# Kernel optimization log

Hardware: AMD Instinct MI355X
Metric: run time of the kernel (lower is better)

## Reference

```python
import jax, jax.numpy as jnp
import numpy as np

B, N, D, K, S = 16, 1024, 256, 16, 512
TEMP = 0.5   # self.temperature, set externally in the repo
EPS = 1e-10


def _gumbel(key, shape):
    u = jax.random.uniform(key, shape, dtype=jnp.float32)
    return -jnp.log(-jnp.log(u + EPS) + EPS)


def setup_inputs() -> dict:
    key = jax.random.key(0)
    k1, k2, k3 = jax.random.split(key, 3)
    return {
        "ze": jax.random.normal(k1, (B, N, D), dtype=jnp.float32),
        "c_logits": jax.random.normal(k2, (B, K), dtype=jnp.float32),
        "books": jax.random.normal(k3, (K, S, D), dtype=jnp.float32),
        "log_param_q": jnp.asarray(np.log(0.5), dtype=jnp.float32),
        "log_param_q_cls": jnp.asarray(np.log(0.5), dtype=jnp.float32),
        "is_train": 1,
    }


def reference(ze, c_logits, books, log_param_q, log_param_q_cls, is_train):
    # training-path forward of GaussianVectorQuantizer
    param_q = 1.0 + jnp.exp(log_param_q)
    precision_q = 0.5 / jnp.clip(param_q, 1e-10)
    param_q_cls = 1.0 + jnp.exp(log_param_q_cls)
    precision_q_cls = 0.5 / jnp.clip(param_q_cls, 1e-10)

    gkey = jax.random.key(42)
    kg1, kg2 = jax.random.split(gkey)

    # gumbel-softmax over clusters: (B, K)
    c_probs = jax.nn.softmax(
        (c_logits * precision_q_cls + _gumbel(kg1, c_logits.shape)) / TEMP, axis=-1
    )

    # pairwise squared distances to every codebook entry of every cluster: (B, N, K, S)
    z2 = jnp.sum(ze * ze, axis=-1)[:, :, None, None]          # (B, N, 1, 1)
    b2 = jnp.sum(books * books, axis=-1)[None, None]          # (1, 1, K, S)
    cross = jnp.einsum('bnd,ksd->bnks', ze, books)            # (B, N, K, S)
    logit_all = -(z2 - 2.0 * cross + b2) * precision_q        # (B, N, K, S)

    # cluster-probability-weighted logits: (B, N, S)
    logits = jnp.einsum('bnks,bk->bns', logit_all, c_probs)

    # gumbel-softmax encodings per cluster, then weighted codebook matmul
    enc = jax.nn.softmax((logit_all + _gumbel(kg2, logit_all.shape)) / TEMP, axis=-1)
    zq = jnp.einsum('bnks,ksd,bk->bnd', enc, books, c_probs)  # (B, N, D)

    prob = jax.nn.softmax(logits, axis=-1)
    log_prob = jax.nn.log_softmax(logits, axis=-1)
    return zq, precision_q, prob, log_prob
```

## Files before the change

kernel.cpp:

```cpp
#include <hip/hip_runtime.h>
#include <cstdint>
#include <cstddef>

#define JAX_PARTITIONABLE 1

namespace {

constexpr int Bsz = 16, Nn = 1024, Dd = 256, Kk = 16, Ss = 512;
constexpr uint32_t BN = (uint32_t)Bsz * Nn;
constexpr int ZQ_SIZE = Bsz * Nn * Dd;
constexpr int PQ_OFF = ZQ_SIZE;
constexpr int PROB_OFF = ZQ_SIZE + 1;
constexpr int BNS = Bsz * Nn * Ss;
constexpr int LP_OFF = PROB_OFF + BNS;

constexpr int WS_CP = 0;
constexpr int WS_B2 = 256;
constexpr int WS_WB2 = WS_B2 + Kk * Ss;
constexpr int WS_WBF = WS_WB2 + Bsz * Ss;
constexpr int WS_BBF = WS_WBF + Bsz * Ss * Dd;
constexpr int WS_BTF = WS_BBF + (Kk * Ss * Dd) / 2;

typedef __attribute__((ext_vector_type(8))) short bf16x8;
typedef __attribute__((ext_vector_type(4))) short short4v;
typedef __attribute__((ext_vector_type(4))) float f32x4;

struct KP { uint32_t a, b; };

__host__ __device__ constexpr KP tf2x32(uint32_t k0, uint32_t k1,
                                        uint32_t x0, uint32_t x1) {
  uint32_t ks[3] = {k0, k1, k0 ^ k1 ^ 0x1BD11BDAu};
  const int rot[2][4] = {{13, 15, 26, 6}, {17, 29, 16, 24}};
  x0 += ks[0];
  x1 += ks[1];
#pragma unroll
  for (int i = 0; i < 5; ++i) {
#pragma unroll
    for (int j = 0; j < 4; ++j) {
      int r = rot[i & 1][j];
      x0 += x1;
      x1 = (x1 << r) | (x1 >> (32 - r));
      x1 ^= x0;
    }
    x0 += ks[(i + 1) % 3];
    x1 += ks[(i + 2) % 3] + (uint32_t)(i + 1);
  }
  return {x0, x1};
}

#if JAX_PARTITIONABLE
constexpr KP KG1 = tf2x32(0u, 42u, 0u, 0u);
constexpr KP KG2 = tf2x32(0u, 42u, 0u, 1u);
#else
constexpr KP KH0 = tf2x32(0u, 42u, 0u, 2u);
constexpr KP KH1 = tf2x32(0u, 42u, 1u, 3u);
constexpr KP KG1 = {KH0.a, KH1.a};
constexpr KP KG2 = {KH0.b, KH1.b};
#endif

__device__ __forceinline__ float jax_gumbel(KP key, uint32_t idx, uint32_t half) {
#if JAX_PARTITIONABLE
  (void)half;
  KP h = tf2x32(key.a, key.b, 0u, idx);
  uint32_t bits = h.a ^ h.b;
#else
  uint32_t lo = idx < half ? idx : idx - half;
  KP h = tf2x32(key.a, key.b, lo, lo + half);
  uint32_t bits = idx < half ? h.a : h.b;
#endif
  float u = __uint_as_float((bits >> 9) | 0x3F800000u) - 1.0f;
  return -__logf(-__logf(u + 1e-10f) + 1e-10f);
}

__device__ __forceinline__ float prec_q(const float* p) {
  return 0.5f / fmaxf(1.0f + expf(p[0]), 1e-10f);
}

__device__ __forceinline__ short f2bf(float x) {
  uint32_t u = __float_as_uint(x);
  uint32_t r = (u + 0x7FFFu + ((u >> 16) & 1u)) >> 16;
  return (short)r;
}

__global__ void __launch_bounds__(256) cprobs_kernel(
    const float* __restrict__ c_logits, const float* __restrict__ lpq,
    const float* __restrict__ lpq_cls, float* __restrict__ ws,
    float* __restrict__ out) {
  __shared__ float sl[256];
  const int t = threadIdx.x;
  const float pqc = prec_q(lpq_cls);
  float g = jax_gumbel(KG1, (uint32_t)t, 128u);
  sl[t] = (c_logits[t] * pqc + g) * 2.0f;
  __syncthreads();
  const int b = t >> 4;
  float m = -3.0e38f;
  for (int j = 0; j < 16; ++j) m = fmaxf(m, sl[b * 16 + j]);
  float sum = 0.f;
  for (int j = 0; j < 16; ++j) sum += expf(sl[b * 16 + j] - m);
  ws[WS_CP + t] = expf(sl[t] - m) / sum;
  if (t == 0) out[PQ_OFF] = prec_q(lpq);
}

__global__ void __launch_bounds__(256) norms_kernel(
    const float* __restrict__ books, float* __restrict__ ws) {
  const int row = blockIdx.x * 4 + (threadIdx.x >> 6);
  const int lane = threadIdx.x & 63;
  float4 v = ((const float4*)(books + (size_t)row * Dd))[lane];
  float s = v.x * v.x + v.y * v.y + v.z * v.z + v.w * v.w;
#pragma unroll
  for (int d = 1; d < 64; d <<= 1) s += __shfl_xor(s, d);
  if (lane == 0) ws[WS_B2 + row] = s;
}

__global__ void __launch_bounds__(256) prep_kernel(
    const float* __restrict__ books, float* __restrict__ ws) {
  __shared__ short tile[16 * 256];
  const int k = blockIdx.x >> 5;
  const int s0 = (blockIdx.x & 31) << 4;
  short* bbf = (short*)(ws + WS_BBF);
  short* btf = (short*)(ws + WS_BTF);
  const int t = threadIdx.x;
#pragma unroll
  for (int i = 0; i < 4; ++i) {
    int idx = t + 256 * i;
    int r = idx >> 6, dq = idx & 63;
    float4 v = ((const float4*)books)[(size_t)(k * Ss + s0 + r) * 64 + dq];
    short4v h = {f2bf(v.x), f2bf(v.y), f2bf(v.z), f2bf(v.w)};
    *(short4v*)&bbf[(size_t)(k * Ss + s0 + r) * 256 + dq * 4] = h;
    *(short4v*)&tile[r * 256 + dq * 4] = h;
  }
  __syncthreads();
  const int d = t;
  short vals[16];
#pragma unroll
  for (int r = 0; r < 16; ++r) vals[r] = tile[r * 256 + d];
  bf16x8 lo, hi;
#pragma unroll
  for (int r = 0; r < 8; ++r) { lo[r] = vals[r]; hi[r] = vals[r + 8]; }
  size_t base = ((size_t)(k * 256 + d)) * 512 + s0;
  *(bf16x8*)&btf[base] = lo;
  *(bf16x8*)&btf[base + 8] = hi;
}

__global__ void __launch_bounds__(256) wbooks_kernel(
    const float* __restrict__ books, float* __restrict__ ws) {
  const int bs = blockIdx.x;
  const int b = bs >> 9, s = bs & 511;
  const int d = threadIdx.x;
  const float* cp = ws + WS_CP + b * 16;
  float acc = 0.f;
#pragma unroll
  for (int k = 0; k < 16; ++k)
    acc = fmaf(cp[k], books[((size_t)(k * Ss + s)) * Dd + d], acc);
  short* wbf = (short*)(ws + WS_WBF);
  wbf[((size_t)(b * Ss + s)) * Dd + d] = f2bf(acc);
  if (d == 0) {
    float a2 = 0.f;
#pragma unroll
    for (int k = 0; k < 16; ++k) a2 = fmaf(cp[k], ws[WS_B2 + k * Ss + s], a2);
    ws[WS_WB2 + b * Ss + s] = a2;
  }
}

__global__ void __launch_bounds__(512, 4) mlogits_kernel(
    const float* __restrict__ ze, const float* __restrict__ lpq,
    const float* __restrict__ ws, float* __restrict__ out) {
  __shared__ short ze_s[32 * 264];
  __shared__ float2 redms[32][9];
  const int b = blockIdx.x >> 5;
  const int n0 = (blockIdx.x & 31) << 5;
  const int t = threadIdx.x;
  const int w = t >> 6, lane = t & 63, c = lane & 15, q = lane >> 4;
  const float pq = prec_q(lpq);
  const short* wbf = (const short*)(ws + WS_WBF);
  const float* wb2 = ws + WS_WB2;

#pragma unroll
  for (int i = 0; i < 4; ++i) {
    int idx = t + 512 * i;
    int r = idx >> 6, dq = idx & 63;
    float4 v = ((const float4*)ze)[(size_t)(b * Nn + n0 + r) * 64 + dq];
    short4v h = {f2bf(v.x), f2bf(v.y), f2bf(v.z), f2bf(v.w)};
    *(short4v*)&ze_s[r * 264 + dq * 4] = h;
  }
  __syncthreads();

  f32x4 acc1[2][4];
#pragma unroll
  for (int rt = 0; rt < 2; ++rt)
#pragma unroll
    for (int st = 0; st < 4; ++st) acc1[rt][st] = (f32x4)(0.f);
  for (int dstep = 0; dstep < 8; ++dstep) {
    bf16x8 a0 = *(const bf16x8*)&ze_s[(c) * 264 + dstep * 32 + q * 8];
    bf16x8 a1 = *(const bf16x8*)&ze_s[(16 + c) * 264 + dstep * 32 + q * 8];
#pragma unroll
    for (int st = 0; st < 4; ++st) {
      bf16x8 bB = *(const bf16x8*)&wbf[((size_t)(b * Ss + w * 64 + st * 16 + c)) * 256 +
                                       dstep * 32 + q * 8];
      acc1[0][st] = __builtin_amdgcn_mfma_f32_16x16x32_bf16(a0, bB, acc1[0][st], 0, 0, 0);
      acc1[1][st] = __builtin_amdgcn_mfma_f32_16x16x32_bf16(a1, bB, acc1[1][st], 0, 0, 0);
    }
  }

  float mx[2][4], sm[2][4];
#pragma unroll
  for (int rt = 0; rt < 2; ++rt)
#pragma unroll
    for (int reg = 0; reg < 4; ++reg) mx[rt][reg] = -3.0e38f;
#pragma unroll
  for (int st = 0; st < 4; ++st) {
    const float wb2v = wb2[b * Ss + w * 64 + st * 16 + c];
#pragma unroll
    for (int rt = 0; rt < 2; ++rt)
#pragma unroll
      for (int reg = 0; reg < 4; ++reg) {
        float v = (2.f * acc1[rt][st][reg] - wb2v) * pq;
        acc1[rt][st][reg] = v;
        mx[rt][reg] = fmaxf(mx[rt][reg], v);
      }
  }
#pragma unroll
  for (int m = 1; m < 16; m <<= 1)
#pragma unroll
    for (int rt = 0; rt < 2; ++rt)
#pragma unroll
      for (int reg = 0; reg < 4; ++reg)
        mx[rt][reg] = fmaxf(mx[rt][reg], __shfl_xor(mx[rt][reg], m));
#pragma unroll
  for (int rt = 0; rt < 2; ++rt)
#pragma unroll
    for (int reg = 0; reg < 4; ++reg) sm[rt][reg] = 0.f;
#pragma unroll
  for (int st = 0; st < 4; ++st)
#pragma unroll
    for (int rt = 0; rt < 2; ++rt)
#pragma unroll
      for (int reg = 0; reg < 4; ++reg)
        sm[rt][reg] += __expf(acc1[rt][st][reg] - mx[rt][reg]);
#pragma unroll
  for (int m = 1; m < 16; m <<= 1)
#pragma unroll
    for (int rt = 0; rt < 2; ++rt)
#pragma unroll
      for (int reg = 0; reg < 4; ++reg) sm[rt][reg] += __shfl_xor(sm[rt][reg], m);
  if (c == 0) {
#pragma unroll
    for (int rt = 0; rt < 2; ++rt)
#pragma unroll
      for (int reg = 0; reg < 4; ++reg)
        redms[rt * 16 + q * 4 + reg][w] = make_float2(mx[rt][reg], sm[rt][reg]);
  }
  __syncthreads();

#pragma unroll
  for (int rt = 0; rt < 2; ++rt)
#pragma unroll
    for (int reg = 0; reg < 4; ++reg) {
      int rl = rt * 16 + q * 4 + reg;
      float M = mx[rt][reg];
#pragma unroll
      for (int w2 = 0; w2 < 8; ++w2) M = fmaxf(M, redms[rl][w2].x);
      float T = 0.f;
#pragma unroll
      for (int w2 = 0; w2 < 8; ++w2)
        T = fmaf(redms[rl][w2].y, __expf(redms[rl][w2].x - M), T);
      const float invT = __builtin_amdgcn_rcpf(T);
      const float lT = __logf(T);
      const size_t base = (size_t)(b * Nn + n0 + rl) * Ss;
#pragma unroll
      for (int st = 0; st < 4; ++st) {
        int s = w * 64 + st * 16 + c;
        float v = acc1[rt][st][reg] - M;
        out[PROB_OFF + base + s] = __expf(v) * invT;
        out[LP_OFF + base + s] = v - lT;
      }
    }
}

__global__ void __launch_bounds__(512, 4) zq_kernel(
    const float* __restrict__ ze, const float* __restrict__ lpq,
    const float* __restrict__ ws, float* __restrict__ out) {
  __shared__ short ze_s[32 * 264];
  __shared__ short enc_s[32 * 520];
  __shared__ float2 redms[32][9];
  __shared__ float cpk[16];

  const int b = blockIdx.x >> 5;
  const int n0 = (blockIdx.x & 31) << 5;
  const int t = threadIdx.x;
  const int w = t >> 6, lane = t & 63, c = lane & 15, q = lane >> 4;
  const float pq = prec_q(lpq);
  const short* bbf = (const short*)(ws + WS_BBF);
  const short* btf = (const short*)(ws + WS_BTF);
  const float* b2p = ws + WS_B2;

  if (t < 16) cpk[t] = ws[WS_CP + b * 16 + t];
#pragma unroll
  for (int i = 0; i < 4; ++i) {
    int idx = t + 512 * i;
    int r = idx >> 6, dq = idx & 63;
    float4 v = ((const float4*)ze)[(size_t)(b * Nn + n0 + r) * 64 + dq];
    short4v h = {f2bf(v.x), f2bf(v.y), f2bf(v.z), f2bf(v.w)};
    *(short4v*)&ze_s[r * 264 + dq * 4] = h;
  }
  __syncthreads();

  f32x4 acc2[2][2];
#pragma unroll
  for (int rt = 0; rt < 2; ++rt)
#pragma unroll
    for (int dt = 0; dt < 2; ++dt) acc2[rt][dt] = (f32x4)(0.f);

  for (int k = 0; k < 16; ++k) {
    f32x4 acc1[2][4];
#pragma unroll
    for (int rt = 0; rt < 2; ++rt)
#pragma unroll
      for (int st = 0; st < 4; ++st) acc1[rt][st] = (f32x4)(0.f);
    for (int dstep = 0; dstep < 8; ++dstep) {
      bf16x8 a0 = *(const bf16x8*)&ze_s[(c) * 264 + dstep * 32 + q * 8];
      bf16x8 a1 = *(const bf16x8*)&ze_s[(16 + c) * 264 + dstep * 32 + q * 8];
#pragma unroll
      for (int st = 0; st < 4; ++st) {
        bf16x8 bB = *(const bf16x8*)&bbf[((size_t)(k * Ss + w * 64 + st * 16 + c)) * 256 +
                                         dstep * 32 + q * 8];
        acc1[0][st] = __builtin_amdgcn_mfma_f32_16x16x32_bf16(a0, bB, acc1[0][st], 0, 0, 0);
        acc1[1][st] = __builtin_amdgcn_mfma_f32_16x16x32_bf16(a1, bB, acc1[1][st], 0, 0, 0);
      }
    }

    float b2v[4];
#pragma unroll
    for (int st = 0; st < 4; ++st) b2v[st] = b2p[k * Ss + w * 64 + st * 16 + c];
    float mx[2][4], sm[2][4];
#pragma unroll
    for (int rt = 0; rt < 2; ++rt)
#pragma unroll
      for (int reg = 0; reg < 4; ++reg) mx[rt][reg] = -3.0e38f;
#pragma unroll
    for (int rt = 0; rt < 2; ++rt)
#pragma unroll
      for (int st = 0; st < 4; ++st)
#pragma unroll
        for (int reg = 0; reg < 4; ++reg) {
          int row = n0 + rt * 16 + q * 4 + reg;
          uint32_t gi = ((uint32_t)(b * Nn + row) * (uint32_t)Kk + (uint32_t)k) * (uint32_t)Ss +
                        (uint32_t)(w * 64 + st * 16 + c);
          float g = jax_gumbel(KG2, gi, 0u);
          float v = ((2.f * acc1[rt][st][reg] - b2v[st]) * pq + g) * 2.f;
          acc1[rt][st][reg] = v;
          mx[rt][reg] = fmaxf(mx[rt][reg], v);
        }
#pragma unroll
    for (int m = 1; m < 16; m <<= 1)
#pragma unroll
      for (int rt = 0; rt < 2; ++rt)
#pragma unroll
        for (int reg = 0; reg < 4; ++reg)
          mx[rt][reg] = fmaxf(mx[rt][reg], __shfl_xor(mx[rt][reg], m));
#pragma unroll
    for (int rt = 0; rt < 2; ++rt)
#pragma unroll
      for (int reg = 0; reg < 4; ++reg) sm[rt][reg] = 0.f;
#pragma unroll
    for (int rt = 0; rt < 2; ++rt)
#pragma unroll
      for (int st = 0; st < 4; ++st)
#pragma unroll
        for (int reg = 0; reg < 4; ++reg) {
          float e = __expf(acc1[rt][st][reg] - mx[rt][reg]);
          acc1[rt][st][reg] = e;
          sm[rt][reg] += e;
        }
#pragma unroll
    for (int m = 1; m < 16; m <<= 1)
#pragma unroll
      for (int rt = 0; rt < 2; ++rt)
#pragma unroll
        for (int reg = 0; reg < 4; ++reg) sm[rt][reg] += __shfl_xor(sm[rt][reg], m);
    if (c == 0) {
#pragma unroll
      for (int rt = 0; rt < 2; ++rt)
#pragma unroll
        for (int reg = 0; reg < 4; ++reg) {
          int rl = rt * 16 + q * 4 + reg;
          redms[rl][w] = make_float2(mx[rt][reg], sm[rt][reg]);
        }
    }
    __syncthreads();

    const float cpv = cpk[k];
#pragma unroll
    for (int rt = 0; rt < 2; ++rt)
#pragma unroll
      for (int reg = 0; reg < 4; ++reg) {
        int rl = rt * 16 + q * 4 + reg;
        float M = mx[rt][reg];
#pragma unroll
        for (int w2 = 0; w2 < 8; ++w2) M = fmaxf(M, redms[rl][w2].x);
        float T = 0.f;
#pragma unroll
        for (int w2 = 0; w2 < 8; ++w2)
          T = fmaf(redms[rl][w2].y, __expf(redms[rl][w2].x - M), T);
        float scale = cpv * __expf(mx[rt][reg] - M) * __builtin_amdgcn_rcpf(T);
#pragma unroll
        for (int st = 0; st < 4; ++st)
          enc_s[rl * 520 + w * 64 + st * 16 + c] = f2bf(acc1[rt][st][reg] * scale);
      }
    __syncthreads();

    for (int ss = 0; ss < 16; ++ss) {
      bf16x8 a0 = *(const bf16x8*)&enc_s[(c) * 520 + ss * 32 + q * 8];
      bf16x8 a1 = *(const bf16x8*)&enc_s[(16 + c) * 520 + ss * 32 + q * 8];
#pragma unroll
      for (int dt = 0; dt < 2; ++dt) {
        bf16x8 bB = *(const bf16x8*)&btf[((size_t)(k * 256 + w * 32 + dt * 16 + c)) * 512 +
                                         ss * 32 + q * 8];
        acc2[0][dt] = __builtin_amdgcn_mfma_f32_16x16x32_bf16(a0, bB, acc2[0][dt], 0, 0, 0);
        acc2[1][dt] = __builtin_amdgcn_mfma_f32_16x16x32_bf16(a1, bB, acc2[1][dt], 0, 0, 0);
      }
    }
  }

#pragma unroll
  for (int rt = 0; rt < 2; ++rt)
#pragma unroll
    for (int dt = 0; dt < 2; ++dt)
#pragma unroll
      for (int reg = 0; reg < 4; ++reg) {
        int row = n0 + rt * 16 + q * 4 + reg;
        int d = w * 32 + dt * 16 + c;
        out[(size_t)(b * Nn + row) * Dd + d] = acc2[rt][dt][reg];
      }
}

}

extern "C" void kernel_launch(void* const* d_in, const int* in_sizes, int n_in,
                              void* d_out, int out_size, void* d_ws, size_t ws_size,
                              hipStream_t stream) {
  (void)in_sizes; (void)n_in; (void)out_size; (void)ws_size;
  const float* ze = (const float*)d_in[0];
  const float* c_logits = (const float*)d_in[1];
  const float* books = (const float*)d_in[2];
  const float* lpq = (const float*)d_in[3];
  const float* lpq_cls = (const float*)d_in[4];
  float* out = (float*)d_out;
  float* ws = (float*)d_ws;

  hipLaunchKernelGGL(cprobs_kernel, dim3(1), dim3(256), 0, stream,
                     c_logits, lpq, lpq_cls, ws, out);
  hipLaunchKernelGGL(norms_kernel, dim3(Kk * Ss / 4), dim3(256), 0, stream, books, ws);
  hipLaunchKernelGGL(prep_kernel, dim3(Kk * 32), dim3(256), 0, stream, books, ws);
  hipLaunchKernelGGL(wbooks_kernel, dim3(Bsz * Ss), dim3(256), 0, stream, books, ws);
  hipLaunchKernelGGL(mlogits_kernel, dim3(Bsz * (Nn / 32)), dim3(512), 0, stream,
                     ze, lpq, ws, out);
  hipLaunchKernelGGL(zq_kernel, dim3(Bsz * (Nn / 32)), dim3(512), 0, stream,
                     ze, lpq, ws, out);
}
```

Measured before the change: 724.2 us.

## Fuse logits and zq kernels into one launch and use exp2 softmax

Merges the logits/prob kernel and the gumbel-softmax zq kernel into a single grid, dispatching by block index so both workloads run concurrently and the launch gap and tail are shared. The zq path also folds temperature, precision and log2e into the constants and uses hardware exp2/log2 for the gumbel noise and softmax, which removes multiplies and conversions per element. In exchange the two block types have unbalanced durations, and the fast log2/exp2 intrinsics may slightly change numerics.

```diff
diff --git a/kernel.cpp b/kernel.cpp
--- a/kernel.cpp
+++ b/kernel.cpp
@@ -21,9 +21,14 @@
 constexpr int WS_BBF = WS_WBF + Bsz * Ss * Dd;
 constexpr int WS_BTF = WS_BBF + (Kk * Ss * Dd) / 2;
 
+constexpr float LOG2E = 1.4426950408889634f;
+
 typedef __attribute__((ext_vector_type(8))) short bf16x8;
 typedef __attribute__((ext_vector_type(4))) short short4v;
 typedef __attribute__((ext_vector_type(4))) float f32x4;
+
+__device__ __forceinline__ float hw_exp2(float x) { return __builtin_amdgcn_exp2f(x); }
+__device__ __forceinline__ float hw_log2(float x) { return __builtin_amdgcn_logf(x); }
 
 struct KP { uint32_t a, b; };
 
@@ -70,6 +75,14 @@
 #endif
   float u = __uint_as_float((bits >> 9) | 0x3F800000u) - 1.0f;
   return -__logf(-__logf(u + 1e-10f) + 1e-10f);
+}
+
+__device__ __forceinline__ float jax_gumbel_w2(KP key, uint32_t idx) {
+  KP h = tf2x32(key.a, key.b, 0u, idx);
+  uint32_t bits = h.a ^ h.b;
+  float u = __uint_as_float((bits >> 9) | 0x3F800000u) - 1.0f;
+  float y = -__logf(u + 1e-10f) + 1e-10f;
+  return -2.0f * hw_log2(y);
 }
 
 __device__ __forceinline__ float prec_q(const float* p) {
@@ -162,122 +175,7 @@
   }
 }
 
-__global__ void __launch_bounds__(512, 4) mlogits_kernel(
-    const float* __restrict__ ze, const float* __restrict__ lpq,
-    const float* __restrict__ ws, float* __restrict__ out) {
-  __shared__ short ze_s[32 * 264];
-  __shared__ float2 redms[32][9];
-  const int b = blockIdx.x >> 5;
-  const int n0 = (blockIdx.x & 31) << 5;
-  const int t = threadIdx.x;
-  const int w = t >> 6, lane = t & 63, c = lane & 15, q = lane >> 4;
-  const float pq = prec_q(lpq);
-  const short* wbf = (const short*)(ws + WS_WBF);
-  const float* wb2 = ws + WS_WB2;
-
-#pragma unroll
-  for (int i = 0; i < 4; ++i) {
-    int idx = t + 512 * i;
-    int r = idx >> 6, dq = idx & 63;
-    float4 v = ((const float4*)ze)[(size_t)(b * Nn + n0 + r) * 64 + dq];
-    short4v h = {f2bf(v.x), f2bf(v.y), f2bf(v.z), f2bf(v.w)};
-    *(short4v*)&ze_s[r * 264 + dq * 4] = h;
-  }
-  __syncthreads();
-
-  f32x4 acc1[2][4];
-#pragma unroll
-  for (int rt = 0; rt < 2; ++rt)
-#pragma unroll
-    for (int st = 0; st < 4; ++st) acc1[rt][st] = (f32x4)(0.f);
-  for (int dstep = 0; dstep < 8; ++dstep) {
-    bf16x8 a0 = *(const bf16x8*)&ze_s[(c) * 264 + dstep * 32 + q * 8];
-    bf16x8 a1 = *(const bf16x8*)&ze_s[(16 + c) * 264 + dstep * 32 + q * 8];
-#pragma unroll
-    for (int st = 0; st < 4; ++st) {
-      bf16x8 bB = *(const bf16x8*)&wbf[((size_t)(b * Ss + w * 64 + st * 16 + c)) * 256 +
-                                       dstep * 32 + q * 8];
-      acc1[0][st] = __builtin_amdgcn_mfma_f32_16x16x32_bf16(a0, bB, acc1[0][st], 0, 0, 0);
-      acc1[1][st] = __builtin_amdgcn_mfma_f32_16x16x32_bf16(a1, bB, acc1[1][st], 0, 0, 0);
-    }
-  }
-
-  float mx[2][4], sm[2][4];
-#pragma unroll
-  for (int rt = 0; rt < 2; ++rt)
-#pragma unroll
-    for (int reg = 0; reg < 4; ++reg) mx[rt][reg] = -3.0e38f;
-#pragma unroll
-  for (int st = 0; st < 4; ++st) {
-    const float wb2v = wb2[b * Ss + w * 64 + st * 16 + c];
-#pragma unroll
-    for (int rt = 0; rt < 2; ++rt)
-#pragma unroll
-      for (int reg = 0; reg < 4; ++reg) {
-        float v = (2.f * acc1[rt][st][reg] - wb2v) * pq;
-        acc1[rt][st][reg] = v;
-        mx[rt][reg] = fmaxf(mx[rt][reg], v);
-      }
-  }
-#pragma unroll
-  for (int m = 1; m < 16; m <<= 1)
-#pragma unroll
-    for (int rt = 0; rt < 2; ++rt)
-#pragma unroll
-      for (int reg = 0; reg < 4; ++reg)
-        mx[rt][reg] = fmaxf(mx[rt][reg], __shfl_xor(mx[rt][reg], m));
-#pragma unroll
-  for (int rt = 0; rt < 2; ++rt)
-#pragma unroll
-    for (int reg = 0; reg < 4; ++reg) sm[rt][reg] = 0.f;
-#pragma unroll
-  for (int st = 0; st < 4; ++st)
-#pragma unroll
-    for (int rt = 0; rt < 2; ++rt)
-#pragma unroll
-      for (int reg = 0; reg < 4; ++reg)
-        sm[rt][reg] += __expf(acc1[rt][st][reg] - mx[rt][reg]);
-#pragma unroll
-  for (int m = 1; m < 16; m <<= 1)
-#pragma unroll
-    for (int rt = 0; rt < 2; ++rt)
-#pragma unroll
-      for (int reg = 0; reg < 4; ++reg) sm[rt][reg] += __shfl_xor(sm[rt][reg], m);
-  if (c == 0) {
-#pragma unroll
-    for (int rt = 0; rt < 2; ++rt)
-#pragma unroll
-      for (int reg = 0; reg < 4; ++reg)
-        redms[rt * 16 + q * 4 + reg][w] = make_float2(mx[rt][reg], sm[rt][reg]);
-  }
-  __syncthreads();
-
-#pragma unroll
-  for (int rt = 0; rt < 2; ++rt)
-#pragma unroll
-    for (int reg = 0; reg < 4; ++reg) {
-      int rl = rt * 16 + q * 4 + reg;
-      float M = mx[rt][reg];
-#pragma unroll
-      for (int w2 = 0; w2 < 8; ++w2) M = fmaxf(M, redms[rl][w2].x);
-      float T = 0.f;
-#pragma unroll
-      for (int w2 = 0; w2 < 8; ++w2)
-        T = fmaf(redms[rl][w2].y, __expf(redms[rl][w2].x - M), T);
-      const float invT = __builtin_amdgcn_rcpf(T);
-      const float lT = __logf(T);
-      const size_t base = (size_t)(b * Nn + n0 + rl) * Ss;
-#pragma unroll
-      for (int st = 0; st < 4; ++st) {
-        int s = w * 64 + st * 16 + c;
-        float v = acc1[rt][st][reg] - M;
-        out[PROB_OFF + base + s] = __expf(v) * invT;
-        out[LP_OFF + base + s] = v - lT;
-      }
-    }
-}
-
-__global__ void __launch_bounds__(512, 4) zq_kernel(
+__global__ void __launch_bounds__(512, 4) fused_kernel(
     const float* __restrict__ ze, const float* __restrict__ lpq,
     const float* __restrict__ ws, float* __restrict__ out) {
   __shared__ short ze_s[32 * 264];
@@ -285,33 +183,174 @@
   __shared__ float2 redms[32][9];
   __shared__ float cpk[16];
 
-  const int b = blockIdx.x >> 5;
-  const int n0 = (blockIdx.x & 31) << 5;
   const int t = threadIdx.x;
   const int w = t >> 6, lane = t & 63, c = lane & 15, q = lane >> 4;
   const float pq = prec_q(lpq);
-  const short* bbf = (const short*)(ws + WS_BBF);
-  const short* btf = (const short*)(ws + WS_BTF);
-  const float* b2p = ws + WS_B2;
-
-  if (t < 16) cpk[t] = ws[WS_CP + b * 16 + t];
-#pragma unroll
-  for (int i = 0; i < 4; ++i) {
-    int idx = t + 512 * i;
-    int r = idx >> 6, dq = idx & 63;
-    float4 v = ((const float4*)ze)[(size_t)(b * Nn + n0 + r) * 64 + dq];
-    short4v h = {f2bf(v.x), f2bf(v.y), f2bf(v.z), f2bf(v.w)};
-    *(short4v*)&ze_s[r * 264 + dq * 4] = h;
-  }
-  __syncthreads();
-
-  f32x4 acc2[2][2];
-#pragma unroll
-  for (int rt = 0; rt < 2; ++rt)
-#pragma unroll
-    for (int dt = 0; dt < 2; ++dt) acc2[rt][dt] = (f32x4)(0.f);
-
-  for (int k = 0; k < 16; ++k) {
+
+  if (blockIdx.x < 512) {
+    const int b = blockIdx.x >> 5;
+    const int n0 = (blockIdx.x & 31) << 5;
+    const short* bbf = (const short*)(ws + WS_BBF);
+    const short* btf = (const short*)(ws + WS_BTF);
+    const float* b2p = ws + WS_B2;
+    const float ca = 4.f * pq * LOG2E;
+    const float cbs = -2.f * pq * LOG2E;
+
+    if (t < 16) cpk[t] = ws[WS_CP + b * 16 + t];
+#pragma unroll
+    for (int i = 0; i < 4; ++i) {
+      int idx = t + 512 * i;
+      int r = idx >> 6, dq = idx & 63;
+      float4 v = ((const float4*)ze)[(size_t)(b * Nn + n0 + r) * 64 + dq];
+      short4v h = {f2bf(v.x), f2bf(v.y), f2bf(v.z), f2bf(v.w)};
+      *(short4v*)&ze_s[r * 264 + dq * 4] = h;
+    }
+    __syncthreads();
+
+    f32x4 acc2[2][2];
+#pragma unroll
+    for (int rt = 0; rt < 2; ++rt)
+#pragma unroll
+      for (int dt = 0; dt < 2; ++dt) acc2[rt][dt] = (f32x4)(0.f);
+
+    for (int k = 0; k < 16; ++k) {
+      f32x4 acc1[2][4];
+#pragma unroll
+      for (int rt = 0; rt < 2; ++rt)
+#pragma unroll
+        for (int st = 0; st < 4; ++st) acc1[rt][st] = (f32x4)(0.f);
+      for (int dstep = 0; dstep < 8; ++dstep) {
+        bf16x8 a0 = *(const bf16x8*)&ze_s[(c) * 264 + dstep * 32 + q * 8];
+        bf16x8 a1 = *(const bf16x8*)&ze_s[(16 + c) * 264 + dstep * 32 + q * 8];
+#pragma unroll
+        for (int st = 0; st < 4; ++st) {
+          bf16x8 bB = *(const bf16x8*)&bbf[((size_t)(k * Ss + w * 64 + st * 16 + c)) * 256 +
+                                           dstep * 32 + q * 8];
+          acc1[0][st] = __builtin_amdgcn_mfma_f32_16x16x32_bf16(a0, bB, acc1[0][st], 0, 0, 0);
+          acc1[1][st] = __builtin_amdgcn_mfma_f32_16x16x32_bf16(a1, bB, acc1[1][st], 0, 0, 0);
+        }
+      }
+
+      float cb[4];
+#pragma unroll
+      for (int st = 0; st < 4; ++st) cb[st] = cbs * b2p[k * Ss + w * 64 + st * 16 + c];
+      float mx[2][4], sm[2][4];
+#pragma unroll
+      for (int rt = 0; rt < 2; ++rt)
+#pragma unroll
+        for (int reg = 0; reg < 4; ++reg) mx[rt][reg] = -3.0e38f;
+#pragma unroll
+      for (int rt = 0; rt < 2; ++rt)
+#pragma unroll
+        for (int st = 0; st < 4; ++st)
+#pragma unroll
+          for (int reg = 0; reg < 4; ++reg) {
+            int row = n0 + rt * 16 + q * 4 + reg;
+            uint32_t gi = ((uint32_t)(b * Nn + row) * (uint32_t)Kk + (uint32_t)k) * (uint32_t)Ss +
+                          (uint32_t)(w * 64 + st * 16 + c);
+            float gw = jax_gumbel_w2(KG2, gi);
+            float v = fmaf(acc1[rt][st][reg], ca, cb[st]) + gw;
+            acc1[rt][st][reg] = v;
+            mx[rt][reg] = fmaxf(mx[rt][reg], v);
+          }
+#pragma unroll
+      for (int m = 1; m < 16; m <<= 1)
+#pragma unroll
+        for (int rt = 0; rt < 2; ++rt)
+#pragma unroll
+          for (int reg = 0; reg < 4; ++reg)
+            mx[rt][reg] = fmaxf(mx[rt][reg], __shfl_xor(mx[rt][reg], m));
+#pragma unroll
+      for (int rt = 0; rt < 2; ++rt)
+#pragma unroll
+        for (int reg = 0; reg < 4; ++reg) sm[rt][reg] = 0.f;
+#pragma unroll
+      for (int rt = 0; rt < 2; ++rt)
+#pragma unroll
+        for (int st = 0; st < 4; ++st)
+#pragma unroll
+          for (int reg = 0; reg < 4; ++reg) {
+            float e = hw_exp2(acc1[rt][st][reg] - mx[rt][reg]);
+            acc1[rt][st][reg] = e;
+            sm[rt][reg] += e;
+          }
+#pragma unroll
+      for (int m = 1; m < 16; m <<= 1)
+#pragma unroll
+        for (int rt = 0; rt < 2; ++rt)
+#pragma unroll
+          for (int reg = 0; reg < 4; ++reg) sm[rt][reg] += __shfl_xor(sm[rt][reg], m);
+      if (c == 0) {
+#pragma unroll
+        for (int rt = 0; rt < 2; ++rt)
+#pragma unroll
+          for (int reg = 0; reg < 4; ++reg) {
+            int rl = rt * 16 + q * 4 + reg;
+            redms[rl][w] = make_float2(mx[rt][reg], sm[rt][reg]);
+          }
+      }
+      __syncthreads();
+
+      const float cpv = cpk[k];
+#pragma unroll
+      for (int rt = 0; rt < 2; ++rt)
+#pragma unroll
+        for (int reg = 0; reg < 4; ++reg) {
+          int rl = rt * 16 + q * 4 + reg;
+          float M = mx[rt][reg];
+#pragma unroll
+          for (int w2 = 0; w2 < 8; ++w2) M = fmaxf(M, redms[rl][w2].x);
+          float T = 0.f;
+#pragma unroll
+          for (int w2 = 0; w2 < 8; ++w2)
+            T = fmaf(redms[rl][w2].y, hw_exp2(redms[rl][w2].x - M), T);
+          float scale = cpv * hw_exp2(mx[rt][reg] - M) * __builtin_amdgcn_rcpf(T);
+#pragma unroll
+          for (int st = 0; st < 4; ++st)
+            enc_s[rl * 520 + w * 64 + st * 16 + c] = f2bf(acc1[rt][st][reg] * scale);
+        }
+      __syncthreads();
+
+      for (int ss = 0; ss < 16; ++ss) {
+        bf16x8 a0 = *(const bf16x8*)&enc_s[(c) * 520 + ss * 32 + q * 8];
+        bf16x8 a1 = *(const bf16x8*)&enc_s[(16 + c) * 520 + ss * 32 + q * 8];
+#pragma unroll
+        for (int dt = 0; dt < 2; ++dt) {
+          bf16x8 bB = *(const bf16x8*)&btf[((size_t)(k * 256 + w * 32 + dt * 16 + c)) * 512 +
+                                           ss * 32 + q * 8];
+          acc2[0][dt] = __builtin_amdgcn_mfma_f32_16x16x32_bf16(a0, bB, acc2[0][dt], 0, 0, 0);
+          acc2[1][dt] = __builtin_amdgcn_mfma_f32_16x16x32_bf16(a1, bB, acc2[1][dt], 0, 0, 0);
+        }
+      }
+    }
+
+#pragma unroll
+    for (int rt = 0; rt < 2; ++rt)
+#pragma unroll
+      for (int dt = 0; dt < 2; ++dt)
+#pragma unroll
+        for (int reg = 0; reg < 4; ++reg) {
+          int row = n0 + rt * 16 + q * 4 + reg;
+          int d = w * 32 + dt * 16 + c;
+          out[(size_t)(b * Nn + row) * Dd + d] = acc2[rt][dt][reg];
+        }
+  } else {
+    const int mbid = blockIdx.x - 512;
+    const int b = mbid >> 5;
+    const int n0 = (mbid & 31) << 5;
+    const short* wbf = (const short*)(ws + WS_WBF);
+    const float* wb2 = ws + WS_WB2;
+
+#pragma unroll
+    for (int i = 0; i < 4; ++i) {
+      int idx = t + 512 * i;
+      int r = idx >> 6, dq = idx & 63;
+      float4 v = ((const float4*)ze)[(size_t)(b * Nn + n0 + r) * 64 + dq];
+      short4v h = {f2bf(v.x), f2bf(v.y), f2bf(v.z), f2bf(v.w)};
+      *(short4v*)&ze_s[r * 264 + dq * 4] = h;
+    }
+    __syncthreads();
+
     f32x4 acc1[2][4];
 #pragma unroll
     for (int rt = 0; rt < 2; ++rt)
@@ -322,35 +361,30 @@
       bf16x8 a1 = *(const bf16x8*)&ze_s[(16 + c) * 264 + dstep * 32 + q * 8];
 #pragma unroll
       for (int st = 0; st < 4; ++st) {
-        bf16x8 bB = *(const bf16x8*)&bbf[((size_t)(k * Ss + w * 64 + st * 16 + c)) * 256 +
+        bf16x8 bB = *(const bf16x8*)&wbf[((size_t)(b * Ss + w * 64 + st * 16 + c)) * 256 +
                                          dstep * 32 + q * 8];
         acc1[0][st] = __builtin_amdgcn_mfma_f32_16x16x32_bf16(a0, bB, acc1[0][st], 0, 0, 0);
         acc1[1][st] = __builtin_amdgcn_mfma_f32_16x16x32_bf16(a1, bB, acc1[1][st], 0, 0, 0);
       }
     }
 
-    float b2v[4];
-#pragma unroll
-    for (int st = 0; st < 4; ++st) b2v[st] = b2p[k * Ss + w * 64 + st * 16 + c];
     float mx[2][4], sm[2][4];
 #pragma unroll
     for (int rt = 0; rt < 2; ++rt)
 #pragma unroll
       for (int reg = 0; reg < 4; ++reg) mx[rt][reg] = -3.0e38f;
 #pragma unroll
-    for (int rt = 0; rt < 2; ++rt)
-#pragma unroll
-      for (int st = 0; st < 4; ++st)
+    for (int st = 0; st < 4; ++st) {
+      const float wb2v = wb2[b * Ss + w * 64 + st * 16 + c];
+#pragma unroll
+      for (int rt = 0; rt < 2; ++rt)
 #pragma unroll
         for (int reg = 0; reg < 4; ++reg) {
-          int row = n0 + rt * 16 + q * 4 + reg;
-          uint32_t gi = ((uint32_t)(b * Nn + row) * (uint32_t)Kk + (uint32_t)k) * (uint32_t)Ss +
-                        (uint32_t)(w * 64 + st * 16 + c);
-          float g = jax_gumbel(KG2, gi, 0u);
-          float v = ((2.f * acc1[rt][st][reg] - b2v[st]) * pq + g) * 2.f;
+          float v = (2.f * acc1[rt][st][reg] - wb2v) * pq;
           acc1[rt][st][reg] = v;
           mx[rt][reg] = fmaxf(mx[rt][reg], v);
         }
+    }
 #pragma unroll
     for (int m = 1; m < 16; m <<= 1)
 #pragma unroll
@@ -363,15 +397,12 @@
 #pragma unroll
       for (int reg = 0; reg < 4; ++reg) sm[rt][reg] = 0.f;
 #pragma unroll
-    for (int rt = 0; rt < 2; ++rt)
-#pragma unroll
-      for (int st = 0; st < 4; ++st)
-#pragma unroll
-        for (int reg = 0; reg < 4; ++reg) {
-          float e = __expf(acc1[rt][st][reg] - mx[rt][reg]);
-          acc1[rt][st][reg] = e;
-          sm[rt][reg] += e;
-        }
+    for (int st = 0; st < 4; ++st)
+#pragma unroll
+      for (int rt = 0; rt < 2; ++rt)
+#pragma unroll
+        for (int reg = 0; reg < 4; ++reg)
+          sm[rt][reg] += __expf(acc1[rt][st][reg] - mx[rt][reg]);
 #pragma unroll
     for (int m = 1; m < 16; m <<= 1)
 #pragma unroll
@@ -382,14 +413,11 @@
 #pragma unroll
       for (int rt = 0; rt < 2; ++rt)
 #pragma unroll
-        for (int reg = 0; reg < 4; ++reg) {
-          int rl = rt * 16 + q * 4 + reg;
-          redms[rl][w] = make_float2(mx[rt][reg], sm[rt][reg]);
-        }
+        for (int reg = 0; reg < 4; ++reg)
+          redms[rt * 16 + q * 4 + reg][w] = make_float2(mx[rt][reg], sm[rt][reg]);
     }
     __syncthreads();
 
-    const float cpv = cpk[k];
 #pragma unroll
     for (int rt = 0; rt < 2; ++rt)
 #pragma unroll
@@ -402,36 +430,18 @@
 #pragma unroll
         for (int w2 = 0; w2 < 8; ++w2)
           T = fmaf(redms[rl][w2].y, __expf(redms[rl][w2].x - M), T);
-        float scale = cpv * __expf(mx[rt][reg] - M) * __builtin_amdgcn_rcpf(T);
-#pragma unroll
-        for (int st = 0; st < 4; ++st)
-          enc_s[rl * 520 + w * 64 + st * 16 + c] = f2bf(acc1[rt][st][reg] * scale);
+        const float invT = __builtin_amdgcn_rcpf(T);
+        const float lT = __logf(T);
+        const size_t base = (size_t)(b * Nn + n0 + rl) * Ss;
+#pragma unroll
+        for (int st = 0; st < 4; ++st) {
+          int s = w * 64 + st * 16 + c;
+          float v = acc1[rt][st][reg] - M;
+          out[PROB_OFF + base + s] = __expf(v) * invT;
+          out[LP_OFF + base + s] = v - lT;
+        }
       }
-    __syncthreads();
-
-    for (int ss = 0; ss < 16; ++ss) {
-      bf16x8 a0 = *(const bf16x8*)&enc_s[(c) * 520 + ss * 32 + q * 8];
-      bf16x8 a1 = *(const bf16x8*)&enc_s[(16 + c) * 520 + ss * 32 + q * 8];
-#pragma unroll
-      for (int dt = 0; dt < 2; ++dt) {
-        bf16x8 bB = *(const bf16x8*)&btf[((size_t)(k * 256 + w * 32 + dt * 16 + c)) * 512 +
-                                         ss * 32 + q * 8];
-        acc2[0][dt] = __builtin_amdgcn_mfma_f32_16x16x32_bf16(a0, bB, acc2[0][dt], 0, 0, 0);
-        acc2[1][dt] = __builtin_amdgcn_mfma_f32_16x16x32_bf16(a1, bB, acc2[1][dt], 0, 0, 0);
-      }
-    }
   }
-
-#pragma unroll
-  for (int rt = 0; rt < 2; ++rt)
-#pragma unroll
-    for (int dt = 0; dt < 2; ++dt)
-#pragma unroll
-      for (int reg = 0; reg < 4; ++reg) {
-        int row = n0 + rt * 16 + q * 4 + reg;
-        int d = w * 32 + dt * 16 + c;
-        out[(size_t)(b * Nn + row) * Dd + d] = acc2[rt][dt][reg];
-      }
 }
 
 }
@@ -453,8 +463,6 @@
   hipLaunchKernelGGL(norms_kernel, dim3(Kk * Ss / 4), dim3(256), 0, stream, books, ws);
   hipLaunchKernelGGL(prep_kernel, dim3(Kk * 32), dim3(256), 0, stream, books, ws);
   hipLaunchKernelGGL(wbooks_kernel, dim3(Bsz * Ss), dim3(256), 0, stream, books, ws);
-  hipLaunchKernelGGL(mlogits_kernel, dim3(Bsz * (Nn / 32)), dim3(512), 0, stream,
+  hipLaunchKernelGGL(fused_kernel, dim3(1024), dim3(512), 0, stream,
                      ze, lpq, ws, out);
-  hipLaunchKernelGGL(zq_kernel, dim3(Bsz * (Nn / 32)), dim3(512), 0, stream,
-                     ze, lpq, ws, out);
-}
+}
```

Result: no change. 724.0 us (-0.0%).
